# Kernel tuning notes

Hardware: AMD Instinct MI355X
Metric: run time of the kernel (lower is better)

The kernel has to match this reference:

```python
import jax, jax.numpy as jnp
import numpy as np


def setup_inputs() -> dict:
    key = jax.random.key(0)
    n, b, E, H, P = 2048, 2, 1024, 16, 16
    ks = jax.random.split(key, 8)
    wscale = 1.0 / np.sqrt(E)  # xavier-ish
    return {
        "query": jax.random.normal(ks[0], (n, b, E), jnp.float32),
        "pquery": jax.random.normal(ks[1], (P, b, E), jnp.float32),
        "Wpq": jax.random.normal(ks[2], (E, E), jnp.float32) * wscale,
        "bpq": jnp.zeros((E,), jnp.float32),
        "Wk": jax.random.normal(ks[3], (E, E), jnp.float32) * wscale,
        "bk": jnp.zeros((E,), jnp.float32),
        "Wv": jax.random.normal(ks[4], (E, E), jnp.float32) * wscale,
        "bv": jnp.zeros((E,), jnp.float32),
        "Wo": jax.random.normal(ks[5], (E, E), jnp.float32) * wscale,
        "bo": jnp.zeros((E,), jnp.float32),
        "num_heads": 16,
    }


def reference(query, pquery, Wpq, bpq, Wk, bk, Wv, bv, Wo, bo, num_heads):
    # query: (n, b, E), pquery: (P, b, E)  [Time x Batch x Channel]
    n, b, E = query.shape
    P = pquery.shape[0]
    H = num_heads
    hd = E // H
    scaling = hd ** -0.5

    # pq projection -> (b, H, P, hd), scaled
    pq = (pquery @ Wpq.T + bpq).reshape(P, b, H, hd).transpose(1, 2, 0, 3) * scaling
    qh = query.reshape(n, b, H, hd)
    # pattn_weights: (b*H, n, P) -- compressed attention logits
    pattn = jnp.einsum('nbhd,bhpd->bhnp', qh, pq).reshape(b * H, n, P)

    def to_bh(x):  # (n,b,E) -> (b*H, n, hd)
        return x.reshape(n, b, H, hd).transpose(1, 2, 0, 3).reshape(b * H, n, hd)

    q = to_bh(query * scaling)
    k = to_bh(query @ Wk.T + bk)
    v = to_bh(query @ Wv.T + bv)

    # Causal prefix softmax over pattn columns. softmax over prefix j<i per
    # column p is exp(pattn[j,p]) / S_i[p] with S_i[p] = sum_{j<i} exp(pattn[j,p]).
    # Shift by per-column global max for stability (softmax shift-invariant).
    m = jnp.max(pattn, axis=1, keepdims=True)
    Eexp = jnp.exp(pattn - m)                       # (BH, n, P)
    S = jnp.cumsum(Eexp, axis=1) - Eexp             # exclusive cumsum (BH, n, P)
    Ssafe = jnp.where(S > 0, S, 1.0)                # row 0 -> zeros numerators anyway

    # Stage 1: attn_weights[i] = q_i @ sum_{j<i} k_j^T softmax(pattn)_j
    KE = k[:, :, :, None] * Eexp[:, :, None, :]     # (BH, n, hd, P)
    Ncum = jnp.cumsum(KE, axis=1) - KE              # exclusive
    attn_weights = jnp.einsum('bnd,bndp->bnp', q, Ncum) / Ssafe  # (BH, n, P)

    aw = jax.nn.softmax(attn_weights, axis=-1)      # (BH, n, P); dropout=0.0

    # Stage 2: attn[i] = aw_i @ sum_{j<i} softmax(pattn)_j v_j^T
    EV = Eexp[:, :, :, None] * v[:, :, None, :]     # (BH, n, P, hd)
    Mcum = jnp.cumsum(EV, axis=1) - EV              # exclusive
    out = jnp.einsum('bnp,bnpd->bnd', aw / Ssafe, Mcum)  # (BH, n, hd)

    attn = out.reshape(b, H, n, hd).transpose(2, 0, 1, 3).reshape(n, b, E)
    attn = attn @ Wo.T + bo

    # need_weights=True, need_head_weights=False -> mean over heads
    aw_avg = aw.reshape(b, H, n, P).mean(axis=1)    # (b, n, P)
    return attn, aw_avg
```

## Files before the change

### kernel.cpp

```cpp
#include <hip/hip_runtime.h>
#include <cstddef>

#define N_TOK 2048
#define BATCH 2
#define EMB   1024
#define NH    16
#define HD    64
#define NP    16
#define BHN   32
#define CHK   64
#define NCHK  32
#define SCALING 0.125f

typedef __attribute__((ext_vector_type(8))) short short8;
typedef __attribute__((ext_vector_type(4))) float f32x4;

typedef __attribute__((address_space(1))) const void gvoid;
typedef __attribute__((address_space(3))) void lvoid;
__device__ __forceinline__ void gload16(const void* g, void* l) {
  __builtin_amdgcn_global_load_lds((gvoid*)g, (lvoid*)l, 16, 0, 0);
}

__device__ __forceinline__ unsigned short f2bf(float f) {
  unsigned u = __float_as_uint(f);
  u += 0x7FFFu + ((u >> 16) & 1u);
  return (unsigned short)(u >> 16);
}
__device__ __forceinline__ float bf2f(unsigned short b) {
  return __uint_as_float((unsigned)b << 16);
}

__global__ __launch_bounds__(256) void prep_pq_kernel(
    const float* __restrict__ query, const float* __restrict__ Wk,
    const float* __restrict__ Wv, const float* __restrict__ Wo,
    const float* __restrict__ bk, const float* __restrict__ bv,
    const float* __restrict__ pquery, const float* __restrict__ Wpq,
    const float* __restrict__ bpq,
    unsigned short* __restrict__ qbf, unsigned short* __restrict__ wkvbf,
    unsigned short* __restrict__ wobf, float* __restrict__ bkv,
    float* __restrict__ pq_s)
{
  const int b = blockIdx.x, t = threadIdx.x;
  if (b < 512) {
    __shared__ float xs[EMB];
    __shared__ float part[4][64];
    const int r = b >> 4, seg = b & 15;
    const int p = r >> 1, ib = r & 1;
    const int el = t & 63, ks = t >> 6;
    const int e = seg * 64 + el;
    for (int l = t; l < EMB; l += 256) xs[l] = pquery[(size_t)r * EMB + l];
    __syncthreads();
    const float* wrow = &Wpq[(size_t)e * EMB + ks * 256];
    const float* xp = &xs[ks * 256];
    float acc = 0.f;
    #pragma unroll 8
    for (int cc = 0; cc < 256; cc += 4) {
      const float4 w4 = *(const float4*)&wrow[cc];
      acc += xp[cc] * w4.x + xp[cc + 1] * w4.y + xp[cc + 2] * w4.z + xp[cc + 3] * w4.w;
    }
    part[ks][el] = acc;
    __syncthreads();
    if (ks == 0) {
      float s = part[0][el] + part[1][el] + part[2][el] + part[3][el];
      s = (s + bpq[e]) * SCALING;
      const int h = e >> 6, d = e & 63;
      pq_s[((size_t)(ib * NH + h) * NP + p) * HD + d] = s;
    }
  } else {
    const int tid = (b - 512) * 256 + t;
    const int NT = 1024 * 256;
    for (int i = tid; i < 1835008; i += NT) {
      const float* src; unsigned short* dst; int off;
      if (i < 1048576)      { src = query; dst = qbf;             off = i; }
      else if (i < 1310720) { src = Wk;    dst = wkvbf;           off = i - 1048576; }
      else if (i < 1572864) { src = Wv;    dst = wkvbf + 1048576; off = i - 1310720; }
      else                  { src = Wo;    dst = wobf;            off = i - 1572864; }
      const float4 v = *(const float4*)&src[(size_t)off * 4];
      ushort4 o;
      o.x = f2bf(v.x); o.y = f2bf(v.y); o.z = f2bf(v.z); o.w = f2bf(v.w);
      *(ushort4*)&dst[(size_t)off * 4] = o;
    }
    if (tid < 512) {
      const int j = tid * 4;
      if (j < 1024) *(float4*)&bkv[j] = *(const float4*)&bk[j];
      else          *(float4*)&bkv[j] = *(const float4*)&bv[j - 1024];
    }
  }
}

__global__ __launch_bounds__(256) void kv_gemm_kernel(
    const unsigned short* __restrict__ Xb, const unsigned short* __restrict__ Wb,
    const float* __restrict__ bias, unsigned short* __restrict__ Y0,
    unsigned short* __restrict__ Y1)
{
  __shared__ unsigned short As[2][4096];
  __shared__ unsigned short Bs[2][2048];
  const int t = threadIdx.x;
  const int L = blockIdx.x;
  const int b = (L & 7) * 128 + (L >> 3);
  const int m0 = (b >> 5) * 128, n0 = (b & 31) * 64;
  const int lane = t & 63, w = t >> 6, wr = w >> 1, wc = w & 1;
  const int lr = lane & 15, lg = lane >> 4;
  const int srow = t >> 2, scol = (t & 3) << 3;
  const unsigned short* xa = &Xb[(size_t)(m0 + srow) * 1024 + scol];
  const unsigned short* xc = &Xb[(size_t)(m0 + srow + 64) * 1024 + scol];
  const unsigned short* wp = &Wb[(size_t)(n0 + srow) * 1024 + scol];
  f32x4 acc[4][2] = {};

  gload16(xa, &As[0][t * 8]);
  gload16(xc, &As[0][2048 + t * 8]);
  gload16(wp, &Bs[0][t * 8]);
  __syncthreads();
  int cur = 0;
  for (int ks = 0; ks < 32; ++ks) {
    if (ks < 31) {
      const int k1 = (ks + 1) * 32;
      gload16(xa + k1, &As[cur ^ 1][t * 8]);
      gload16(xc + k1, &As[cur ^ 1][2048 + t * 8]);
      gload16(wp + k1, &Bs[cur ^ 1][t * 8]);
    }
    short8 av[4], bv[2];
    #pragma unroll
    for (int m = 0; m < 4; ++m) av[m] = *(const short8*)&As[cur][(wr * 64 + m * 16 + lr) * 32 + lg * 8];
    #pragma unroll
    for (int n = 0; n < 2; ++n) bv[n] = *(const short8*)&Bs[cur][(wc * 32 + n * 16 + lr) * 32 + lg * 8];
    #pragma unroll
    for (int m = 0; m < 4; ++m)
      #pragma unroll
      for (int n = 0; n < 2; ++n)
        acc[m][n] = __builtin_amdgcn_mfma_f32_16x16x32_bf16(av[m], bv[n], acc[m][n], 0, 0, 0);
    __syncthreads();
    cur ^= 1;
  }

  unsigned short* dst = (n0 < 1024) ? Y0 : Y1;
  #pragma unroll
  for (int n = 0; n < 2; ++n) {
    const int gcol = n0 + wc * 32 + n * 16 + lr;
    const float bcol = bias[gcol];
    const int lcol = gcol & 1023;
    #pragma unroll
    for (int m = 0; m < 4; ++m) {
      const int row0 = m0 + wr * 64 + m * 16 + lg * 4;
      #pragma unroll
      for (int q = 0; q < 4; ++q)
        dst[(size_t)(row0 + q) * 1024 + lcol] = f2bf(acc[m][n][q] + bcol);
    }
  }
}

__global__ __launch_bounds__(256) void pattn_totals_kernel(
    const unsigned short* __restrict__ qbf, const float* __restrict__ pq_s,
    const unsigned short* __restrict__ Kbf, const unsigned short* __restrict__ Vbf,
    unsigned short* __restrict__ peb, float* __restrict__ Tk, float* __restrict__ Tv,
    float* __restrict__ Tsc)
{
  const int c = blockIdx.x, bh = blockIdx.y;
  const int ib = bh >> 4, h = bh & 15;
  const int t = threadIdx.x;
  const int i0 = c * CHK;
  const int lane = t & 63, w = t >> 6;
  const int lr = lane & 15, lg = lane >> 4;

  __shared__ float qs[CHK][68];
  __shared__ float ps[NP][68];
  __shared__ unsigned short KT[64][80];
  __shared__ unsigned short VT[64][80];
  __shared__ unsigned short EbT[16][80];
  __shared__ float Ef[64][20];
  __shared__ float tspart[4][16];

  for (int l = t; l < CHK * 8; l += 256) {
    const int i = l >> 3, d8 = (l & 7) << 3;
    const uint4 u = *(const uint4*)&qbf[((size_t)(i0 + i) * BATCH + ib) * EMB + h * HD + d8];
    const unsigned short* qq = (const unsigned short*)&u;
    #pragma unroll
    for (int e = 0; e < 8; ++e) qs[i][d8 + e] = bf2f(qq[e]);
  }
  {
    const int pp = t >> 4, d4 = (t & 15) << 2;
    *(float4*)&ps[pp][d4] = *(const float4*)&pq_s[((size_t)bh * NP + pp) * HD + d4];
  }
  #pragma unroll
  for (int it = 0; it < 2; ++it) {
    const int task = t + it * 256;
    const int j = task & 63, dg = task >> 6;
    const size_t g = ((size_t)(i0 + j) * BATCH + ib) * EMB + h * HD + dg * 8;
    const uint4 ku = *(const uint4*)&Kbf[g];
    const uint4 vu = *(const uint4*)&Vbf[g];
    const unsigned short* kk = (const unsigned short*)&ku;
    const unsigned short* vv = (const unsigned short*)&vu;
    #pragma unroll
    for (int e = 0; e < 8; ++e) { KT[dg * 8 + e][j] = kk[e]; VT[dg * 8 + e][j] = vv[e]; }
  }
  __syncthreads();

  {
    const int p = t & 15, ig = t >> 4;
    #pragma unroll
    for (int rep = 0; rep < 4; ++rep) {
      const int i = rep * 16 + ig;
      float acc = 0.f;
      for (int d = 0; d < HD; ++d) acc += qs[i][d] * ps[p][d];
      const float e = expf(acc);
      const unsigned short eb = f2bf(e);
      peb[(size_t)bh * (N_TOK * NP) + (size_t)(i0 + i) * NP + p] = eb;
      Ef[i][p] = e;
      EbT[p][i] = eb;
    }
  }
  __syncthreads();

  if (t < 64) {
    const int p = t & 15, qq = t >> 4;
    float s = 0.f;
    #pragma unroll
    for (int jj = 0; jj < 16; ++jj) s += Ef[qq * 16 + jj][p];
    tspart[qq][p] = s;
  }

  short8 ae0 = *(const short8*)&EbT[lr][lg * 8];
  short8 ae1 = *(const short8*)&EbT[lr][32 + lg * 8];
  const size_t tb = (size_t)(bh * NCHK + c) * 1024;

  {
    f32x4 ka = {};
    short8 bk0 = *(const short8*)&KT[w * 16 + lr][lg * 8];
    short8 bk1 = *(const short8*)&KT[w * 16 + lr][32 + lg * 8];
    ka = __builtin_amdgcn_mfma_f32_16x16x32_bf16(ae0, bk0, ka, 0, 0, 0);
    ka = __builtin_amdgcn_mfma_f32_16x16x32_bf16(ae1, bk1, ka, 0, 0, 0);
    #pragma unroll
    for (int q = 0; q < 4; ++q) Tk[tb + (lg * 4 + q) * 64 + w * 16 + lr] = ka[q];
  }
  {
    f32x4 va = {};
    short8 av0 = *(const short8*)&VT[w * 16 + lr][lg * 8];
    short8 av1 = *(const short8*)&VT[w * 16 + lr][32 + lg * 8];
    va = __builtin_amdgcn_mfma_f32_16x16x32_bf16(av0, ae0, va, 0, 0, 0);
    va = __builtin_amdgcn_mfma_f32_16x16x32_bf16(av1, ae1, va, 0, 0, 0);
    #pragma unroll
    for (int q = 0; q < 4; ++q) Tv[tb + (w * 16 + lg * 4 + q) * 16 + lr] = va[q];
  }
  __syncthreads();
  if (t < 16)
    Tsc[(size_t)(bh * NCHK + c) * 16 + t] =
        tspart[0][t] + tspart[1][t] + tspart[2][t] + tspart[3][t];
}

__global__ __launch_bounds__(256) void chunk_scan_kernel(
    float* __restrict__ Tk, float* __restrict__ Tv, float* __restrict__ Ts)
{
  const int bh = blockIdx.x, y = blockIdx.y, t = threadIdx.x;
  const int slot = y * 256 + t;
  float* arr = (slot < 1024) ? Tk : Tv;
  const int e = slot & 1023;
  const size_t base = (size_t)bh * (NCHK * 1024) + e;
  float v[NCHK];
  #pragma unroll
  for (int c = 0; c < NCHK; ++c) v[c] = arr[base + (size_t)c * 1024];
  float run = 0.f;
  #pragma unroll
  for (int c = 0; c < NCHK; ++c) { arr[base + (size_t)c * 1024] = run; run += v[c]; }
  if (y == 7 && t < 16) {
    const size_t sb = (size_t)bh * (NCHK * 16) + t;
    float s[NCHK];
    #pragma unroll
    for (int c = 0; c < NCHK; ++c) s[c] = Ts[sb + c * 16];
    float rs = 0.f;
    #pragma unroll
    for (int c = 0; c < NCHK; ++c) { Ts[sb + c * 16] = rs; rs += s[c]; }
  }
}

__global__ __launch_bounds__(256) void attn_mfma_kernel(
    const unsigned short* __restrict__ qbf, const unsigned short* __restrict__ Kbf,
    const unsigned short* __restrict__ Vbf, const unsigned short* __restrict__ peb,
    const float* __restrict__ Tk, const float* __restrict__ Tv,
    const float* __restrict__ Ts, float* __restrict__ aw_buf,
    unsigned short* __restrict__ outpre)
{
  const int c = blockIdx.x, bh = blockIdx.y;
  const int ib = bh >> 4, h = bh & 15;
  const int t = threadIdx.x;
  const int i0 = c * CHK;
  const int lane = t & 63, w = t >> 6;
  const int ws = w * 16;
  const int lr = lane & 15, lg = lane >> 4;
  const int nsl = (w >> 1) + 1;

  __shared__ unsigned short Kb[64][80];
  __shared__ unsigned short VT[64][80];
  __shared__ unsigned short Ab[64][80];
  __shared__ unsigned short Eb[64][40];
  __shared__ unsigned short EbT[16][80];
  __shared__ unsigned short Nbt[16][80];
  __shared__ unsigned short Mbt[64][40];
  __shared__ unsigned short Gb[64][40];
  __shared__ float Sbf[16];

  const size_t qg = ((size_t)(i0 + ws + lr) * BATCH + ib) * EMB + h * HD;
  short8 avq0 = *(const short8*)&qbf[qg + lg * 8];
  short8 avq1 = *(const short8*)&qbf[qg + 32 + lg * 8];

  #pragma unroll
  for (int it = 0; it < 2; ++it) {
    const int task = t + it * 256;
    const int i = task >> 3, d0 = (task & 7) << 3;
    *(uint4*)&Kb[i][d0] = *(const uint4*)&Kbf[((size_t)(i0 + i) * BATCH + ib) * EMB + h * HD + d0];
  }
  #pragma unroll
  for (int it = 0; it < 2; ++it) {
    const int task = t + it * 256;
    const int j = task & 63, dg = task >> 6;
    const size_t g = ((size_t)(i0 + j) * BATCH + ib) * EMB + h * HD + dg * 8;
    const uint4 vu = *(const uint4*)&Vbf[g];
    const unsigned short* vv = (const unsigned short*)&vu;
    #pragma unroll
    for (int e = 0; e < 8; ++e) VT[dg * 8 + e][j] = vv[e];
  }
  {
    const int j = t >> 2, p0 = (t & 3) << 2;
    const ushort4 e4 = *(const ushort4*)&peb[(size_t)bh * (N_TOK * NP) + (size_t)(i0 + j) * NP + p0];
    Eb[j][p0] = e4.x; Eb[j][p0 + 1] = e4.y; Eb[j][p0 + 2] = e4.z; Eb[j][p0 + 3] = e4.w;
    Eb[j][p0 + 16] = 0; Eb[j][p0 + 17] = 0; Eb[j][p0 + 18] = 0; Eb[j][p0 + 19] = 0;
    EbT[p0][j] = e4.x; EbT[p0 + 1][j] = e4.y; EbT[p0 + 2][j] = e4.z; EbT[p0 + 3][j] = e4.w;
  }
  {
    const int p = t >> 4, d0 = (t & 15) << 2;
    const float4 v = *(const float4*)&Tk[(size_t)(bh * NCHK + c) * 1024 + p * 64 + d0];
    Nbt[p][d0] = f2bf(v.x); Nbt[p][d0 + 1] = f2bf(v.y);
    Nbt[p][d0 + 2] = f2bf(v.z); Nbt[p][d0 + 3] = f2bf(v.w);
  }
  {
    const int d = t >> 2, p0 = (t & 3) << 2;
    const float4 v = *(const float4*)&Tv[(size_t)(bh * NCHK + c) * 1024 + d * 16 + p0];
    Mbt[d][p0] = f2bf(v.x); Mbt[d][p0 + 1] = f2bf(v.y);
    Mbt[d][p0 + 2] = f2bf(v.z); Mbt[d][p0 + 3] = f2bf(v.w);
    Mbt[d][p0 + 16] = 0; Mbt[d][p0 + 17] = 0; Mbt[d][p0 + 18] = 0; Mbt[d][p0 + 19] = 0;
  }
  if (t < 16) Sbf[t] = Ts[(size_t)(bh * NCHK + c) * 16 + t];
  __syncthreads();

  f32x4 sacc[4] = {};
  for (int n = 0; n <= w; ++n) {
    short8 bk0 = *(const short8*)&Kb[n * 16 + lr][lg * 8];
    short8 bk1 = *(const short8*)&Kb[n * 16 + lr][32 + lg * 8];
    sacc[n] = __builtin_amdgcn_mfma_f32_16x16x32_bf16(avq0, bk0, sacc[n], 0, 0, 0);
    sacc[n] = __builtin_amdgcn_mfma_f32_16x16x32_bf16(avq1, bk1, sacc[n], 0, 0, 0);
  }
  #pragma unroll
  for (int q = 0; q < 4; ++q)
    if (lr >= lg * 4 + q) sacc[w][q] = 0.f;
  for (int n = 0; n < 2 * nsl; ++n)
    #pragma unroll
    for (int q = 0; q < 4; ++q)
      Ab[ws + lg * 4 + q][n * 16 + lr] = f2bf(sacc[n][q]);

  short8 bve0 = *(const short8*)&EbT[lr][lg * 8];
  short8 bve1 = *(const short8*)&EbT[lr][32 + lg * 8];

  f32x4 wacc = {};
  {
    short8 bn0 = *(const short8*)&Nbt[lr][lg * 8];
    short8 bn1 = *(const short8*)&Nbt[lr][32 + lg * 8];
    wacc = __builtin_amdgcn_mfma_f32_16x16x32_bf16(avq0, bn0, wacc, 0, 0, 0);
    wacc = __builtin_amdgcn_mfma_f32_16x16x32_bf16(avq1, bn1, wacc, 0, 0, 0);
  }
  for (int ks = 0; ks < nsl; ++ks) {
    short8 aa = *(const short8*)&Ab[ws + lr][ks * 32 + lg * 8];
    wacc = __builtin_amdgcn_mfma_f32_16x16x32_bf16(aa, ks ? bve1 : bve0, wacc, 0, 0, 0);
  }
  const float s0 = Sbf[lr];
  f32x4 scacc = {s0, s0, s0, s0};
  for (int ks = 0; ks < nsl; ++ks) {
    const int jb = ks * 32 + lg * 8;
    const int irow = ws + lr;
    short8 ones;
    #pragma unroll
    for (int e = 0; e < 8; ++e) ones[e] = (short)((jb + e < irow) ? 0x3F80 : 0);
    scacc = __builtin_amdgcn_mfma_f32_16x16x32_bf16(ones, ks ? bve1 : bve0, scacc, 0, 0, 0);
  }

  const size_t awbase = (size_t)bh * (N_TOK * NP) + (size_t)i0 * NP;
  #pragma unroll
  for (int q = 0; q < 4; ++q) {
    const int il = lg * 4 + q;
    const float ssum = scacc[q];
    const float ssafe = (ssum > 0.f) ? ssum : 1.f;
    const float wv = SCALING * wacc[q] / ssafe;
    float m = wv;
    #pragma unroll
    for (int off = 1; off < 16; off <<= 1) m = fmaxf(m, __shfl_xor(m, off, 64));
    const float e = expf(wv - m);
    float ss = e;
    #pragma unroll
    for (int off = 1; off < 16; off <<= 1) ss += __shfl_xor(ss, off, 64);
    const float aw = e / ss;
    aw_buf[awbase + (size_t)(ws + il) * NP + lr] = aw;
    const float g = aw / ssafe;
    Gb[ws + il][lr] = f2bf(g);
    Gb[ws + il][lr + 16] = 0;
  }

  short8 ga = *(const short8*)&Gb[ws + lr][lg * 8];
  f32x4 bacc[4] = {};
  for (int n = 0; n <= w; ++n) {
    short8 be = *(const short8*)&Eb[n * 16 + lr][lg * 8];
    bacc[n] = __builtin_amdgcn_mfma_f32_16x16x32_bf16(ga, be, bacc[n], 0, 0, 0);
  }
  #pragma unroll
  for (int q = 0; q < 4; ++q)
    if (lr >= lg * 4 + q) bacc[w][q] = 0.f;
  for (int n = 0; n < 2 * nsl; ++n)
    #pragma unroll
    for (int q = 0; q < 4; ++q)
      Ab[ws + lg * 4 + q][n * 16 + lr] = f2bf(bacc[n][q]);

  f32x4 oacc[4] = {};
  #pragma unroll
  for (int dn = 0; dn < 4; ++dn) {
    short8 bm = *(const short8*)&Mbt[dn * 16 + lr][lg * 8];
    oacc[dn] = __builtin_amdgcn_mfma_f32_16x16x32_bf16(ga, bm, oacc[dn], 0, 0, 0);
  }
  for (int ks = 0; ks < nsl; ++ks) {
    short8 ab = *(const short8*)&Ab[ws + lr][ks * 32 + lg * 8];
    #pragma unroll
    for (int dn = 0; dn < 4; ++dn) {
      short8 bv = *(const short8*)&VT[dn * 16 + lr][ks * 32 + lg * 8];
      oacc[dn] = __builtin_amdgcn_mfma_f32_16x16x32_bf16(ab, bv, oacc[dn], 0, 0, 0);
    }
  }

  #pragma unroll
  for (int dn = 0; dn < 4; ++dn)
    #pragma unroll
    for (int q = 0; q < 4; ++q) {
      const int i = ws + lg * 4 + q;
      const int d = dn * 16 + lr;
      outpre[((size_t)(i0 + i) * BATCH + ib) * EMB + h * HD + d] = f2bf(oacc[dn][q]);
    }
}

__global__ __launch_bounds__(256) void o_aw_kernel(
    const unsigned short* __restrict__ Xb, const unsigned short* __restrict__ Wb,
    const float* __restrict__ bias, float* __restrict__ Yf,
    const float* __restrict__ aw_buf, float* __restrict__ out_aw)
{
  __shared__ unsigned short As[2][4096];
  __shared__ unsigned short Bs[2][2048];
  const int L = blockIdx.x, t = threadIdx.x;
  if (L < 512) {
    const int b = (L & 7) * 64 + (L >> 3);
    const int m0 = (b >> 4) * 128, n0 = (b & 15) * 64;
    const int lane = t & 63, w = t >> 6, wr = w >> 1, wc = w & 1;
    const int lr = lane & 15, lg = lane >> 4;
    const int srow = t >> 2, scol = (t & 3) << 3;
    const unsigned short* xa = &Xb[(size_t)(m0 + srow) * 1024 + scol];
    const unsigned short* xc = &Xb[(size_t)(m0 + srow + 64) * 1024 + scol];
    const unsigned short* wp = &Wb[(size_t)(n0 + srow) * 1024 + scol];
    f32x4 acc[4][2] = {};

    gload16(xa, &As[0][t * 8]);
    gload16(xc, &As[0][2048 + t * 8]);
    gload16(wp, &Bs[0][t * 8]);
    __syncthreads();
    int cur = 0;
    for (int ks = 0; ks < 32; ++ks) {
      if (ks < 31) {
        const int k1 = (ks + 1) * 32;
        gload16(xa + k1, &As[cur ^ 1][t * 8]);
        gload16(xc + k1, &As[cur ^ 1][2048 + t * 8]);
        gload16(wp + k1, &Bs[cur ^ 1][t * 8]);
      }
      short8 av[4], bv[2];
      #pragma unroll
      for (int m = 0; m < 4; ++m) av[m] = *(const short8*)&As[cur][(wr * 64 + m * 16 + lr) * 32 + lg * 8];
      #pragma unroll
      for (int n = 0; n < 2; ++n) bv[n] = *(const short8*)&Bs[cur][(wc * 32 + n * 16 + lr) * 32 + lg * 8];
      #pragma unroll
      for (int m = 0; m < 4; ++m)
        #pragma unroll
        for (int n = 0; n < 2; ++n)
          acc[m][n] = __builtin_amdgcn_mfma_f32_16x16x32_bf16(av[m], bv[n], acc[m][n], 0, 0, 0);
      __syncthreads();
      cur ^= 1;
    }
    #pragma unroll
    for (int n = 0; n < 2; ++n) {
      const int gcol = n0 + wc * 32 + n * 16 + lr;
      const float bcol = bias[gcol];
      #pragma unroll
      for (int m = 0; m < 4; ++m) {
        const int row0 = m0 + wr * 64 + m * 16 + lg * 4;
        #pragma unroll
        for (int q = 0; q < 4; ++q)
          Yf[(size_t)(row0 + q) * 1024 + gcol] = acc[m][n][q] + bcol;
      }
    }
  } else {
    const int idx = (L - 512) * 256 + t;
    const int p = idx & 15;
    const int i = (idx >> 4) & 2047;
    const int ib = idx >> 15;
    float s = 0.f;
    for (int hh = 0; hh < NH; ++hh)
      s += aw_buf[((size_t)(ib * NH + hh) * N_TOK + i) * NP + p];
    out_aw[idx] = s * (1.f / 16.f);
  }
}

extern "C" void kernel_launch(void* const* d_in, const int* in_sizes, int n_in,
                              void* d_out, int out_size, void* d_ws, size_t ws_size,
                              hipStream_t stream) {
  const float* query  = (const float*)d_in[0];
  const float* pquery = (const float*)d_in[1];
  const float* Wpq    = (const float*)d_in[2];
  const float* bpq    = (const float*)d_in[3];
  const float* Wk     = (const float*)d_in[4];
  const float* bk     = (const float*)d_in[5];
  const float* Wv     = (const float*)d_in[6];
  const float* bv     = (const float*)d_in[7];
  const float* Wo     = (const float*)d_in[8];
  const float* bo     = (const float*)d_in[9];
  float* out = (float*)d_out;
  float* ws  = (float*)d_ws;

  float* pq_s   = ws;
  float* aw_buf = pq_s + 32768;
  float* Tk     = aw_buf + 1048576;
  float* Tv     = Tk + 1048576;
  float* Ts     = Tv + 1048576;
  float* bkv    = Ts + 16384;
  unsigned short* peb   = (unsigned short*)(bkv + 2048);
  unsigned short* qbf   = peb + 1048576;
  unsigned short* Kbf   = qbf + 4194304;
  unsigned short* Vbf   = Kbf + 4194304;
  unsigned short* wkvbf = Vbf + 4194304;
  unsigned short* wobf  = wkvbf + 2097152;
  unsigned short* opbf  = wobf + 1048576;

  prep_pq_kernel<<<1536, 256, 0, stream>>>(query, Wk, Wv, Wo, bk, bv, pquery, Wpq, bpq,
                                           qbf, wkvbf, wobf, bkv, pq_s);
  kv_gemm_kernel<<<1024, 256, 0, stream>>>(qbf, wkvbf, bkv, Kbf, Vbf);
  pattn_totals_kernel<<<dim3(NCHK, BHN), 256, 0, stream>>>(qbf, pq_s, Kbf, Vbf,
                                                           peb, Tk, Tv, Ts);
  chunk_scan_kernel<<<dim3(BHN, 8), 256, 0, stream>>>(Tk, Tv, Ts);
  attn_mfma_kernel<<<dim3(NCHK, BHN), 256, 0, stream>>>(qbf, Kbf, Vbf, peb, Tk, Tv, Ts,
                                                        aw_buf, opbf);
  o_aw_kernel<<<768, 256, 0, stream>>>(opbf, wobf, bo, out, aw_buf, out + 4194304);
}
```

Measured before the change: 115.8 us.

## Widen KV GEMM tile to 128x128 and compute pattn logits with MFMA

```diff
diff --git a/kernel.cpp b/kernel.cpp
--- a/kernel.cpp
+++ b/kernel.cpp
@@ -38,7 +38,7 @@
     const float* __restrict__ bpq,
     unsigned short* __restrict__ qbf, unsigned short* __restrict__ wkvbf,
     unsigned short* __restrict__ wobf, float* __restrict__ bkv,
-    float* __restrict__ pq_s)
+    unsigned short* __restrict__ pq_sb)
 {
   const int b = blockIdx.x, t = threadIdx.x;
   if (b < 512) {
@@ -64,7 +64,7 @@
       float s = part[0][el] + part[1][el] + part[2][el] + part[3][el];
       s = (s + bpq[e]) * SCALING;
       const int h = e >> 6, d = e & 63;
-      pq_s[((size_t)(ib * NH + h) * NP + p) * HD + d] = s;
+      pq_sb[((size_t)(ib * NH + h) * NP + p) * HD + d] = f2bf(s);
     }
   } else {
     const int tid = (b - 512) * 256 + t;
@@ -94,22 +94,24 @@
     unsigned short* __restrict__ Y1)
 {
   __shared__ unsigned short As[2][4096];
-  __shared__ unsigned short Bs[2][2048];
+  __shared__ unsigned short Bs[2][4096];
   const int t = threadIdx.x;
   const int L = blockIdx.x;
-  const int b = (L & 7) * 128 + (L >> 3);
-  const int m0 = (b >> 5) * 128, n0 = (b & 31) * 64;
+  const int b = (L & 7) * 64 + (L >> 3);
+  const int m0 = (b >> 4) * 128, n0 = (b & 15) * 128;
   const int lane = t & 63, w = t >> 6, wr = w >> 1, wc = w & 1;
   const int lr = lane & 15, lg = lane >> 4;
   const int srow = t >> 2, scol = (t & 3) << 3;
   const unsigned short* xa = &Xb[(size_t)(m0 + srow) * 1024 + scol];
-  const unsigned short* xc = &Xb[(size_t)(m0 + srow + 64) * 1024 + scol];
+  const unsigned short* xc = xa + (size_t)64 * 1024;
   const unsigned short* wp = &Wb[(size_t)(n0 + srow) * 1024 + scol];
-  f32x4 acc[4][2] = {};
+  const unsigned short* wq = wp + (size_t)64 * 1024;
+  f32x4 acc[4][4] = {};
 
   gload16(xa, &As[0][t * 8]);
   gload16(xc, &As[0][2048 + t * 8]);
   gload16(wp, &Bs[0][t * 8]);
+  gload16(wq, &Bs[0][2048 + t * 8]);
   __syncthreads();
   int cur = 0;
   for (int ks = 0; ks < 32; ++ks) {
@@ -118,16 +120,17 @@
       gload16(xa + k1, &As[cur ^ 1][t * 8]);
       gload16(xc + k1, &As[cur ^ 1][2048 + t * 8]);
       gload16(wp + k1, &Bs[cur ^ 1][t * 8]);
-    }
-    short8 av[4], bv[2];
+      gload16(wq + k1, &Bs[cur ^ 1][2048 + t * 8]);
+    }
+    short8 av[4], bv[4];
     #pragma unroll
     for (int m = 0; m < 4; ++m) av[m] = *(const short8*)&As[cur][(wr * 64 + m * 16 + lr) * 32 + lg * 8];
     #pragma unroll
-    for (int n = 0; n < 2; ++n) bv[n] = *(const short8*)&Bs[cur][(wc * 32 + n * 16 + lr) * 32 + lg * 8];
+    for (int n = 0; n < 4; ++n) bv[n] = *(const short8*)&Bs[cur][(wc * 64 + n * 16 + lr) * 32 + lg * 8];
     #pragma unroll
     for (int m = 0; m < 4; ++m)
       #pragma unroll
-      for (int n = 0; n < 2; ++n)
+      for (int n = 0; n < 4; ++n)
         acc[m][n] = __builtin_amdgcn_mfma_f32_16x16x32_bf16(av[m], bv[n], acc[m][n], 0, 0, 0);
     __syncthreads();
     cur ^= 1;
@@ -135,8 +138,8 @@
 
   unsigned short* dst = (n0 < 1024) ? Y0 : Y1;
   #pragma unroll
-  for (int n = 0; n < 2; ++n) {
-    const int gcol = n0 + wc * 32 + n * 16 + lr;
+  for (int n = 0; n < 4; ++n) {
+    const int gcol = n0 + wc * 64 + n * 16 + lr;
     const float bcol = bias[gcol];
     const int lcol = gcol & 1023;
     #pragma unroll
@@ -150,7 +153,7 @@
 }
 
 __global__ __launch_bounds__(256) void pattn_totals_kernel(
-    const unsigned short* __restrict__ qbf, const float* __restrict__ pq_s,
+    const unsigned short* __restrict__ qbf, const unsigned short* __restrict__ pq_sb,
     const unsigned short* __restrict__ Kbf, const unsigned short* __restrict__ Vbf,
     unsigned short* __restrict__ peb, float* __restrict__ Tk, float* __restrict__ Tv,
     float* __restrict__ Tsc)
@@ -161,26 +164,14 @@
   const int i0 = c * CHK;
   const int lane = t & 63, w = t >> 6;
   const int lr = lane & 15, lg = lane >> 4;
-
-  __shared__ float qs[CHK][68];
-  __shared__ float ps[NP][68];
+  const int wrow = w * 16;
+
   __shared__ unsigned short KT[64][80];
   __shared__ unsigned short VT[64][80];
   __shared__ unsigned short EbT[16][80];
   __shared__ float Ef[64][20];
   __shared__ float tspart[4][16];
 
-  for (int l = t; l < CHK * 8; l += 256) {
-    const int i = l >> 3, d8 = (l & 7) << 3;
-    const uint4 u = *(const uint4*)&qbf[((size_t)(i0 + i) * BATCH + ib) * EMB + h * HD + d8];
-    const unsigned short* qq = (const unsigned short*)&u;
-    #pragma unroll
-    for (int e = 0; e < 8; ++e) qs[i][d8 + e] = bf2f(qq[e]);
-  }
-  {
-    const int pp = t >> 4, d4 = (t & 15) << 2;
-    *(float4*)&ps[pp][d4] = *(const float4*)&pq_s[((size_t)bh * NP + pp) * HD + d4];
-  }
   #pragma unroll
   for (int it = 0; it < 2; ++it) {
     const int task = t + it * 256;
@@ -193,20 +184,25 @@
     #pragma unroll
     for (int e = 0; e < 8; ++e) { KT[dg * 8 + e][j] = kk[e]; VT[dg * 8 + e][j] = vv[e]; }
   }
-  __syncthreads();
-
-  {
-    const int p = t & 15, ig = t >> 4;
-    #pragma unroll
-    for (int rep = 0; rep < 4; ++rep) {
-      const int i = rep * 16 + ig;
-      float acc = 0.f;
-      for (int d = 0; d < HD; ++d) acc += qs[i][d] * ps[p][d];
-      const float e = expf(acc);
+
+  {
+    const size_t qg = ((size_t)(i0 + wrow + lr) * BATCH + ib) * EMB + h * HD;
+    short8 avq0 = *(const short8*)&qbf[qg + lg * 8];
+    short8 avq1 = *(const short8*)&qbf[qg + 32 + lg * 8];
+    const size_t pb = (size_t)bh * 1024 + (size_t)lr * 64;
+    short8 bp0 = *(const short8*)&pq_sb[pb + lg * 8];
+    short8 bp1 = *(const short8*)&pq_sb[pb + 32 + lg * 8];
+    f32x4 lacc = {};
+    lacc = __builtin_amdgcn_mfma_f32_16x16x32_bf16(avq0, bp0, lacc, 0, 0, 0);
+    lacc = __builtin_amdgcn_mfma_f32_16x16x32_bf16(avq1, bp1, lacc, 0, 0, 0);
+    #pragma unroll
+    for (int q = 0; q < 4; ++q) {
+      const int i = wrow + lg * 4 + q;
+      const float e = expf(lacc[q]);
       const unsigned short eb = f2bf(e);
-      peb[(size_t)bh * (N_TOK * NP) + (size_t)(i0 + i) * NP + p] = eb;
-      Ef[i][p] = e;
-      EbT[p][i] = eb;
+      peb[(size_t)bh * (N_TOK * NP) + (size_t)(i0 + i) * NP + lr] = eb;
+      Ef[i][lr] = e;
+      EbT[lr][i] = eb;
     }
   }
   __syncthreads();
@@ -525,13 +521,13 @@
   float* out = (float*)d_out;
   float* ws  = (float*)d_ws;
 
-  float* pq_s   = ws;
-  float* aw_buf = pq_s + 32768;
+  float* aw_buf = ws;
   float* Tk     = aw_buf + 1048576;
   float* Tv     = Tk + 1048576;
   float* Ts     = Tv + 1048576;
   float* bkv    = Ts + 16384;
-  unsigned short* peb   = (unsigned short*)(bkv + 2048);
+  unsigned short* pq_sb = (unsigned short*)(bkv + 2048);
+  unsigned short* peb   = pq_sb + 32768;
   unsigned short* qbf   = peb + 1048576;
   unsigned short* Kbf   = qbf + 4194304;
   unsigned short* Vbf   = Kbf + 4194304;
@@ -540,9 +536,9 @@
   unsigned short* opbf  = wobf + 1048576;
 
   prep_pq_kernel<<<1536, 256, 0, stream>>>(query, Wk, Wv, Wo, bk, bv, pquery, Wpq, bpq,
-                                           qbf, wkvbf, wobf, bkv, pq_s);
-  kv_gemm_kernel<<<1024, 256, 0, stream>>>(qbf, wkvbf, bkv, Kbf, Vbf);
-  pattn_totals_kernel<<<dim3(NCHK, BHN), 256, 0, stream>>>(qbf, pq_s, Kbf, Vbf,
+                                           qbf, wkvbf, wobf, bkv, pq_sb);
+  kv_gemm_kernel<<<512, 256, 0, stream>>>(qbf, wkvbf, bkv, Kbf, Vbf);
+  pattn_totals_kernel<<<dim3(NCHK, BHN), 256, 0, stream>>>(qbf, pq_sb, Kbf, Vbf,
                                                            peb, Tk, Tv, Ts);
   chunk_scan_kernel<<<dim3(BHN, 8), 256, 0, stream>>>(Tk, Tv, Ts);
   attn_mfma_kernel<<<dim3(NCHK, BHN), 256, 0, stream>>>(qbf, Kbf, Vbf, peb, Tk, Tv, Ts,
```

Result: faster. 110.8 us (-4.4%).
